# Optimization experiments

Hardware: AMD Instinct MI355X
Metric: run time of the kernel (lower is better)

## Reference

```python
import jax, jax.numpy as jnp
import numpy as np

B, S, D, H, DH, G, C, FF = 4, 4096, 768, 12, 64, 64, 256, 3072


def _ln(x, g, b):
    m = x.mean(-1, keepdims=True)
    v = ((x - m) ** 2).mean(-1, keepdims=True)
    return (x - m) * jax.lax.rsqrt(v + 1e-5) * g + b


def setup_inputs() -> dict:
    key = jax.random.key(0)
    ks = jax.random.split(key, 20)
    w = lambda k, shape: jax.random.normal(k, shape, jnp.float32) * 0.02
    inp = dict(
        cur_input=jax.random.normal(ks[0], (B, S, D), jnp.float32),
        prevLayerOutput=jax.random.normal(ks[1], (B, S, D), jnp.float32),
        classVector=jax.random.normal(ks[2], (B, C), jnp.float32),
        rand_idx=jax.random.randint(ks[3], (B, G), 0, S),
        # self-attention (rand+global) projections
        Wq=w(ks[4], (D, D)), bq=jnp.zeros(D), Wk=w(ks[5], (D, D)), bk=jnp.zeros(D),
        Wv=w(ks[6], (D, D)), bv=jnp.zeros(D), Wo=w(ks[7], (D, D)), bo=jnp.zeros(D),
        g1=jnp.ones(D), b1=jnp.zeros(D),
        # cross-attention over class vector (k/v feature dim is 1 after unsqueeze(-1))
        Wqc=w(ks[8], (D, D)), bqc=jnp.zeros(D), Wkc=w(ks[9], (1, D)), bkc=jnp.zeros(D),
        Wvc=w(ks[10], (1, D)), bvc=jnp.zeros(D), Woc=w(ks[11], (D, D)), boc=jnp.zeros(D),
        g2=jnp.ones(D), b2=jnp.zeros(D),
        # feed-forward
        W1=w(ks[12], (D, FF)), bf1=jnp.zeros(FF), W2=w(ks[13], (FF, D)), bf2=jnp.zeros(D),
        g3=jnp.ones(D), b3=jnp.zeros(D),
    )
    return inp


def reference(cur_input, prevLayerOutput, classVector, rand_idx,
              Wq, bq, Wk, bk, Wv, bv, Wo, bo, g1, b1,
              Wqc, bqc, Wkc, bkc, Wvc, bvc, Woc, boc, g2, b2,
              W1, bf1, W2, bf2, g3, b3):
    scale = np.float32(1.0 / np.sqrt(DH))
    # ---- masked multi-head self attention over global + random tokens ----
    q = (cur_input @ Wq + bq).reshape(B, S, H, DH)
    k = (prevLayerOutput @ Wk + bk).reshape(B, S, H, DH)
    v = (prevLayerOutput @ Wv + bv).reshape(B, S, H, DH)
    sel = jnp.concatenate([jnp.broadcast_to(jnp.arange(G), (B, G)), rand_idx], axis=1)  # [B,2G]
    idx = jnp.broadcast_to(sel[:, :, None, None], (B, 2 * G, H, DH))
    ksel = jnp.take_along_axis(k, idx, axis=1)  # [B,2G,H,DH]
    vsel = jnp.take_along_axis(v, idx, axis=1)
    scores = jnp.einsum('bshd,bkhd->bhsk', q, ksel) * scale  # [B,H,S,2G]
    mask = sel[:, None, None, :] <= jnp.arange(S)[None, None, :, None]  # causal wrt key position
    scores = jnp.where(mask, scores, jnp.float32(-1e9))
    attn = jax.nn.softmax(scores, axis=-1)
    o = jnp.einsum('bhsk,bkhd->bshd', attn, vsel).reshape(B, S, D) @ Wo + bo
    x1 = _ln(cur_input + o, g1, b1)
    # ---- cross attention over class vector (kv seq = C, kv feat = 1) ----
    cv = classVector[:, :, None]  # [B,C,1]
    qc = (x1 @ Wqc + bqc).reshape(B, S, H, DH)
    kc = (cv @ Wkc + bkc).reshape(B, C, H, DH)
    vc = (cv @ Wvc + bvc).reshape(B, C, H, DH)
    sc = jnp.einsum('bshd,bchd->bhsc', qc, kc) * scale
    ac = jax.nn.softmax(sc, axis=-1)
    oc = jnp.einsum('bhsc,bchd->bshd', ac, vc).reshape(B, S, D) @ Woc + boc
    x2 = _ln(x1 + oc, g2, b2)
    # ---- feed forward ----
    ff = jax.nn.relu(x2 @ W1 + bf1) @ W2 + bf2
    return _ln(x2 + ff, g3, b3)
```

## Files before the change

kernel.cpp:

```cpp
#include <hip/hip_runtime.h>
#include <hip/hip_bf16.h>

#define B_ 4
#define S_ 4096
#define D_ 768
#define H_ 12
#define DH_ 64
#define G_ 64
#define C_ 256
#define FF_ 3072

typedef __attribute__((ext_vector_type(8))) short bf16x8;
typedef __attribute__((ext_vector_type(4))) float f32x4;
typedef unsigned short u16;

__device__ __forceinline__ float bfu2f(u16 u) {
    return __uint_as_float((unsigned)u << 16);
}

__device__ __forceinline__ void gload16(const __hip_bfloat16* g, __hip_bfloat16* l) {
    __builtin_amdgcn_global_load_lds(
        (__attribute__((address_space(1))) void*)(void*)const_cast<__hip_bfloat16*>(g),
        (__attribute__((address_space(3))) void*)(void*)l,
        16, 0, 0);
}

__global__ __launch_bounds__(512, 2) void gemm256(
    const u16* __restrict__ A, const u16* __restrict__ Bt,
    const float* __restrict__ bias, u16* __restrict__ Cb,
    int M, int N, int K, int flags)
{
    __shared__ __attribute__((aligned(16))) u16 Ah[2][2][128 * 64];
    __shared__ __attribute__((aligned(16))) u16 Bh[2][2][128 * 64];

    const int tid = threadIdx.x;
    const int lane = tid & 63, w = tid >> 6;
    const int wm = w >> 2, wn = w & 3;
    const int r = lane & 15, qd = lane >> 4;

    int lin = blockIdx.y * gridDim.x + blockIdx.x;
    int nwg = gridDim.x * gridDim.y;
    int cpx = nwg >> 3;
    int swz = (lin & 7) * cpx + (lin >> 3);
    int bm = (swz / gridDim.x) * 256;
    int bn = (swz % gridDim.x) * 256;

    const int srow = tid >> 3;
    const int scol = ((tid & 7) ^ (srow & 7)) * 8;
    const int sdst = tid * 8;

#define STG_A(c, h, kt) { \
    const u16* s_ = A + (size_t)(bm + (h) * 128 + srow) * K + ((kt) << 6) + scol; \
    gload16((const __hip_bfloat16*)s_, (__hip_bfloat16*)&Ah[c][h][sdst]); \
    gload16((const __hip_bfloat16*)(s_ + (size_t)64 * K), (__hip_bfloat16*)&Ah[c][h][sdst + 4096]); }
#define STG_B(c, h, kt) { \
    const u16* s_ = Bt + (size_t)(bn + (h) * 128 + srow) * K + ((kt) << 6) + scol; \
    gload16((const __hip_bfloat16*)s_, (__hip_bfloat16*)&Bh[c][h][sdst]); \
    gload16((const __hip_bfloat16*)(s_ + (size_t)64 * K), (__hip_bfloat16*)&Bh[c][h][sdst + 4096]); }

#define GRAN(kk) (((((kk) << 2) + qd) ^ (r & 7)) * 8)
#define READS_AF(c, mb) { \
    _Pragma("unroll") for (int m = 0; m < 4; ++m) { \
        const u16* p_ = &Ah[c][wm][((mb + m) * 16 + r) * 64]; \
        af[m][0] = *(const bf16x8*)(p_ + GRAN(0)); \
        af[m][1] = *(const bf16x8*)(p_ + GRAN(1)); } }
#define READS_BF(dst, c, nb) { \
    _Pragma("unroll") for (int n = 0; n < 2; ++n) { \
        const u16* p_ = &Bh[c][wn >> 1][((wn & 1) * 64 + (nb + n) * 16 + r) * 64]; \
        dst[n][0] = *(const bf16x8*)(p_ + GRAN(0)); \
        dst[n][1] = *(const bf16x8*)(p_ + GRAN(1)); } }
#define QMFMA(mb, nb, bfx) { \
    __builtin_amdgcn_s_setprio(1); \
    _Pragma("unroll") for (int kk = 0; kk < 2; ++kk) \
    _Pragma("unroll") for (int m = 0; m < 4; ++m) \
    _Pragma("unroll") for (int n = 0; n < 2; ++n) \
        acc[mb + m][nb + n] = __builtin_amdgcn_mfma_f32_16x16x32_bf16( \
            af[m][kk], bfx[n][kk], acc[mb + m][nb + n], 0, 0, 0); \
    __builtin_amdgcn_s_setprio(0); }
#define BAR() __builtin_amdgcn_s_barrier()
#define LGKM0() asm volatile("s_waitcnt lgkmcnt(0)" ::: "memory")

    f32x4 acc[8][4] = {};
    const int NT = K >> 6;
    const int J = NT >> 1;

    STG_A(0, 0, 0) STG_A(0, 1, 0) STG_B(0, 0, 0) STG_B(0, 1, 0)
    STG_B(1, 0, 1) STG_B(1, 1, 1)
    asm volatile("s_waitcnt vmcnt(4)" ::: "memory");
    BAR();

    bf16x8 af[4][2], bf0[2][2], bf1[2][2];

    for (int j = 0; j < J; ++j) {
        const int to1 = 2 * j + 1;
        const int te2 = 2 * j + 2;
        const int to3 = 2 * j + 3;
        const bool pf = (j < J - 1);

        READS_AF(0, 0) READS_BF(bf0, 0, 0)
        STG_A(1, 0, to1)
        BAR(); LGKM0();
        QMFMA(0, 0, bf0)
        BAR();
        READS_BF(bf1, 0, 2)
        STG_A(1, 1, to1)
        BAR(); LGKM0();
        QMFMA(0, 2, bf1)
        BAR();
        READS_AF(0, 4)
        if (pf) { STG_B(0, 0, te2) }
        BAR(); LGKM0();
        QMFMA(4, 2, bf1)
        BAR();
        if (pf) { STG_B(0, 1, te2) }
        BAR();
        QMFMA(4, 0, bf0)
        if (pf) asm volatile("s_waitcnt vmcnt(4)" ::: "memory");
        else    asm volatile("s_waitcnt vmcnt(0)" ::: "memory");
        BAR();
        READS_AF(1, 0) READS_BF(bf0, 1, 0)
        if (pf) { STG_A(0, 0, te2) }
        BAR(); LGKM0();
        QMFMA(0, 0, bf0)
        BAR();
        READS_BF(bf1, 1, 2)
        if (pf) { STG_A(0, 1, te2) }
        BAR(); LGKM0();
        QMFMA(0, 2, bf1)
        BAR();
        READS_AF(1, 4)
        if (pf) { STG_B(1, 0, to3) }
        BAR(); LGKM0();
        QMFMA(4, 2, bf1)
        BAR();
        if (pf) { STG_B(1, 1, to3) }
        BAR();
        QMFMA(4, 0, bf0)
        if (pf) {
            asm volatile("s_waitcnt vmcnt(4)" ::: "memory");
            BAR();
        }
    }

#pragma unroll
    for (int m = 0; m < 8; ++m) {
        int row0 = bm + wm * 128 + m * 16 + qd * 4;
#pragma unroll
        for (int n = 0; n < 4; ++n) {
            int col = bn + wn * 64 + n * 16 + r;
            float bv = (flags & 1) ? bias[col] : 0.0f;
#pragma unroll
            for (int i = 0; i < 4; ++i) {
                float v = acc[m][n][i] + bv;
                if (flags & 2) v = fmaxf(v, 0.0f);
                __hip_bfloat16 ob = __float2bfloat16(v);
                Cb[(size_t)(row0 + i) * N + col] = *(u16*)&ob;
            }
        }
    }
#undef STG_A
#undef STG_B
#undef GRAN
#undef READS_AF
#undef READS_BF
#undef QMFMA
#undef BAR
#undef LGKM0
}

__global__ __launch_bounds__(256) void gemm_mfma(
    const __hip_bfloat16* __restrict__ A, const __hip_bfloat16* __restrict__ Bt,
    const float* __restrict__ bias, float* __restrict__ Cf,
    __hip_bfloat16* __restrict__ Cb,
    int M, int N, int K, int lda, int ldbt, int flags)
{
    __shared__ __hip_bfloat16 As[2][128 * 32];
    __shared__ __hip_bfloat16 Bs[2][128 * 32];

    const int t = threadIdx.x;
    const int lane = t & 63;
    const int wave = t >> 6;
    const int wr = wave >> 1, wc = wave & 1;
    const int qd = lane >> 4, r = lane & 15;

    int lin = blockIdx.y * gridDim.x + blockIdx.x;
    int nwg = gridDim.x * gridDim.y;
    int cpx = nwg >> 3;
    int swz = (lin & 7) * cpx + (lin >> 3);
    int bm = (swz / gridDim.x) * 128;
    int bn = (swz % gridDim.x) * 128;

    const int srow = lane >> 2;
    const int scol = (lane & 3) * 8;
    const __hip_bfloat16* gA0 = A + (size_t)(bm + wave * 32 + srow) * lda + scol;
    const __hip_bfloat16* gA1 = gA0 + (size_t)16 * lda;
    const __hip_bfloat16* gB0 = Bt + (size_t)(bn + wave * 32 + srow) * ldbt + scol;
    const __hip_bfloat16* gB1 = gB0 + (size_t)16 * ldbt;

    f32x4 acc[4][4] = {};

    gload16(gA0, &As[0][wave * 1024]);
    gload16(gA1, &As[0][wave * 1024 + 512]);
    gload16(gB0, &Bs[0][wave * 1024]);
    gload16(gB1, &Bs[0][wave * 1024 + 512]);
    __syncthreads();

    int cur = 0;
    for (int k0 = 0; k0 < K; k0 += 32, cur ^= 1) {
        if (k0 + 32 < K) {
            int kn = k0 + 32, nb = cur ^ 1;
            gload16(gA0 + kn, &As[nb][wave * 1024]);
            gload16(gA1 + kn, &As[nb][wave * 1024 + 512]);
            gload16(gB0 + kn, &Bs[nb][wave * 1024]);
            gload16(gB1 + kn, &Bs[nb][wave * 1024 + 512]);
        }
        bf16x8 afr[4], bfr[4];
#pragma unroll
        for (int m = 0; m < 4; ++m)
            afr[m] = *(const bf16x8*)&As[cur][(wr * 64 + m * 16 + r) * 32 + qd * 8];
#pragma unroll
        for (int n = 0; n < 4; ++n)
            bfr[n] = *(const bf16x8*)&Bs[cur][(wc * 64 + n * 16 + r) * 32 + qd * 8];
#pragma unroll
        for (int m = 0; m < 4; ++m)
#pragma unroll
            for (int n = 0; n < 4; ++n)
                acc[m][n] = __builtin_amdgcn_mfma_f32_16x16x32_bf16(
                    afr[m], bfr[n], acc[m][n], 0, 0, 0);
        __syncthreads();
    }

#pragma unroll
    for (int m = 0; m < 4; ++m) {
        int row0 = bm + wr * 64 + m * 16 + qd * 4;
#pragma unroll
        for (int n = 0; n < 4; ++n) {
            int col = bn + wc * 64 + n * 16 + r;
            float bv = (flags & 1) ? bias[col] : 0.0f;
#pragma unroll
            for (int i = 0; i < 4; ++i) {
                float v = acc[m][n][i] + bv;
                if (flags & 2) v = fmaxf(v, 0.0f);
                size_t off = (size_t)(row0 + i) * N + col;
                if (flags & 4) v += Cf[off];
                if (flags & 8) Cb[off] = __float2bfloat16(v);
                else           Cf[off] = v;
            }
        }
    }
}

__global__ __launch_bounds__(256) void conv_bf16(const float* __restrict__ in,
                                                 __hip_bfloat16* __restrict__ out,
                                                 int n8)
{
    int i = blockIdx.x * 256 + threadIdx.x;
    if (i >= n8) return;
    const float4* p = (const float4*)(in + (size_t)i * 8);
    float4 v0 = p[0], v1 = p[1];
    __hip_bfloat16 o[8] = {
        __float2bfloat16(v0.x), __float2bfloat16(v0.y),
        __float2bfloat16(v0.z), __float2bfloat16(v0.w),
        __float2bfloat16(v1.x), __float2bfloat16(v1.y),
        __float2bfloat16(v1.z), __float2bfloat16(v1.w)};
    *(uint4*)(out + (size_t)i * 8) = *(const uint4*)o;
}

__global__ __launch_bounds__(256) void transp_all(
    const float* __restrict__ Wq, const float* __restrict__ Wo,
    const float* __restrict__ Wk, const float* __restrict__ Wv,
    const float* __restrict__ W1, const float* __restrict__ W2,
    __hip_bfloat16* __restrict__ Wqt, __hip_bfloat16* __restrict__ Wot,
    __hip_bfloat16* __restrict__ Wkt, __hip_bfloat16* __restrict__ Wvt,
    __hip_bfloat16* __restrict__ W1t, __hip_bfloat16* __restrict__ W2t)
{
    int tile = blockIdx.x;
    const float* W; __hip_bfloat16* Wt; int K, N;
    if (tile < 2304) {
        int w = tile / 576; tile -= w * 576;
        K = 768; N = 768;
        W  = (w == 0) ? Wq : (w == 1) ? Wo : (w == 2) ? Wk : Wv;
        Wt = (w == 0) ? Wqt : (w == 1) ? Wot : (w == 2) ? Wkt : Wvt;
    } else if (tile < 4608) { tile -= 2304; K = 768; N = 3072; W = W1; Wt = W1t; }
    else                    { tile -= 4608; K = 3072; N = 768; W = W2; Wt = W2t; }
    int ntx = N >> 5;
    int k0 = (tile / ntx) * 32, n0 = (tile % ntx) * 32;
    __shared__ float s[32][33];
    int tx = threadIdx.x & 31, ty = threadIdx.x >> 5;
#pragma unroll
    for (int i = 0; i < 4; ++i)
        s[ty + i * 8][tx] = W[(size_t)(k0 + ty + i * 8) * N + n0 + tx];
    __syncthreads();
#pragma unroll
    for (int i = 0; i < 4; ++i)
        Wt[(size_t)(n0 + ty + i * 8) * K + k0 + tx] =
            __float2bfloat16(s[tx][ty + i * 8]);
}

__global__ void gather_kernel(const float* __restrict__ prev,
                              const int* __restrict__ rand_idx,
                              __hip_bfloat16* __restrict__ Pselb,
                              int* __restrict__ sel)
{
    int j = blockIdx.x;
    int b = j >> 7, i = j & 127;
    int sv = (i < 64) ? i : rand_idx[b * G_ + (i - 64)];
    if (threadIdx.x == 0) sel[j] = sv;
    const float* src = prev + ((size_t)(b * S_ + sv)) * D_;
    __hip_bfloat16* dst = Pselb + (size_t)j * D_;
    for (int d = threadIdx.x; d < D_; d += blockDim.x)
        dst[d] = __float2bfloat16(src[d]);
}

__global__ __launch_bounds__(256) void attn3_kernel(
    const u16* __restrict__ qb, const u16* __restrict__ kb,
    const u16* __restrict__ vb, const int* __restrict__ sel,
    u16* __restrict__ out)
{
    const int bh = blockIdx.y;
    const int b = bh / H_, h = bh % H_;
    const int s0 = blockIdx.x * 256;
    const int t = threadIdx.x;
    const int w = t >> 6, lane = t & 63;
    const int r = lane & 15, qd = lane >> 4;

    __shared__ u16 Vt[64][136];
    __shared__ u16 Plds[4][32][136];
    __shared__ int ssel[128];

    {
        int key0 = t >> 4;
        int d0 = (t & 15) * 4;
        for (int kk = key0; kk < 128; kk += 16) {
            ushort4 v = *(const ushort4*)(vb + (size_t)(b * 128 + kk) * D_ + h * 64 + d0);
            Vt[d0 + 0][kk] = v.x; Vt[d0 + 1][kk] = v.y;
            Vt[d0 + 2][kk] = v.z; Vt[d0 + 3][kk] = v.w;
        }
        if (t < 128) ssel[t] = sel[b * 128 + t];
    }
    __syncthreads();

    int selv[8];
#pragma unroll
    for (int n = 0; n < 8; ++n) selv[n] = ssel[n * 16 + r];

    for (int pass = 0; pass < 2; ++pass) {
        const int sbase = s0 + w * 64 + pass * 32;
        f32x4 accs[2][8] = {};

#pragma unroll
        for (int ks = 0; ks < 2; ++ks) {
            bf16x8 af[2];
#pragma unroll
            for (int m = 0; m < 2; ++m)
                af[m] = *(const bf16x8*)(qb + (size_t)(b * S_ + sbase + m * 16 + r) * D_ + h * 64 + ks * 32 + qd * 8);
#pragma unroll
            for (int n = 0; n < 8; ++n) {
                bf16x8 bfv = *(const bf16x8*)(kb + (size_t)(b * 128 + n * 16 + r) * D_ + h * 64 + ks * 32 + qd * 8);
#pragma unroll
                for (int m = 0; m < 2; ++m)
                    accs[m][n] = __builtin_amdgcn_mfma_f32_16x16x32_bf16(
                        af[m], bfv, accs[m][n], 0, 0, 0);
            }
        }

#pragma unroll
        for (int m = 0; m < 2; ++m) {
#pragma unroll
            for (int i = 0; i < 4; ++i) {
                int srow = sbase + m * 16 + qd * 4 + i;
                float pm = -3e38f;
#pragma unroll
                for (int n = 0; n < 8; ++n) {
                    float sc = accs[m][n][i] * 0.125f;
                    if (selv[n] > srow) sc = -1e9f;
                    accs[m][n][i] = sc;
                    pm = fmaxf(pm, sc);
                }
#pragma unroll
                for (int off = 1; off < 16; off <<= 1)
                    pm = fmaxf(pm, __shfl_xor(pm, off, 64));
                float ps = 0.f;
#pragma unroll
                for (int n = 0; n < 8; ++n) {
                    float e = __expf(accs[m][n][i] - pm);
                    accs[m][n][i] = e;
                    ps += e;
                }
#pragma unroll
                for (int off = 1; off < 16; off <<= 1)
                    ps += __shfl_xor(ps, off, 64);
                float inv = 1.0f / ps;
#pragma unroll
                for (int n = 0; n < 8; ++n)
                    accs[m][n][i] *= inv;
            }
        }

#pragma unroll
        for (int m = 0; m < 2; ++m)
#pragma unroll
            for (int n = 0; n < 8; ++n)
#pragma unroll
                for (int i = 0; i < 4; ++i) {
                    __hip_bfloat16 pb = __float2bfloat16(accs[m][n][i]);
                    Plds[w][m * 16 + qd * 4 + i][n * 16 + r] = *(u16*)&pb;
                }

        f32x4 acco[2][4] = {};
#pragma unroll
        for (int ks = 0; ks < 4; ++ks) {
            bf16x8 pa[2];
#pragma unroll
            for (int m = 0; m < 2; ++m)
                pa[m] = *(const bf16x8*)&Plds[w][m * 16 + r][ks * 32 + qd * 8];
#pragma unroll
            for (int nd = 0; nd < 4; ++nd) {
                bf16x8 bv = *(const bf16x8*)&Vt[nd * 16 + r][ks * 32 + qd * 8];
#pragma unroll
                for (int m = 0; m < 2; ++m)
                    acco[m][nd] = __builtin_amdgcn_mfma_f32_16x16x32_bf16(
                        pa[m], bv, acco[m][nd], 0, 0, 0);
            }
        }

#pragma unroll
        for (int m = 0; m < 2; ++m)
#pragma unroll
            for (int nd = 0; nd < 4; ++nd)
#pragma unroll
                for (int i = 0; i < 4; ++i) {
                    __hip_bfloat16 ob = __float2bfloat16(acco[m][nd][i]);
                    out[(size_t)(b * S_ + sbase + m * 16 + qd * 4 + i) * D_ + h * 64 + nd * 16 + r] = *(u16*)&ob;
                }
    }
}

__global__ __launch_bounds__(192) void addln_bb(
    const u16* __restrict__ xa, const u16* __restrict__ xb,
    const float* __restrict__ g, const float* __restrict__ beta,
    float* __restrict__ out)
{
    const int row = blockIdx.x;
    const int t = threadIdx.x;
    const ushort4 a = ((const ushort4*)(xa + (size_t)row * D_))[t];
    const ushort4 b4 = ((const ushort4*)(xb + (size_t)row * D_))[t];
    float v[4] = {bfu2f(a.x) + bfu2f(b4.x), bfu2f(a.y) + bfu2f(b4.y),
                  bfu2f(a.z) + bfu2f(b4.z), bfu2f(a.w) + bfu2f(b4.w)};
    float sum = v[0] + v[1] + v[2] + v[3];
#pragma unroll
    for (int off = 1; off < 64; off <<= 1) sum += __shfl_xor(sum, off, 64);
    __shared__ float r1[3], r2[3];
    int wv = t >> 6, ln = t & 63;
    if (ln == 0) r1[wv] = sum;
    __syncthreads();
    float mean = (r1[0] + r1[1] + r1[2]) * (1.0f / 768.0f);
    float sq = 0.f;
#pragma unroll
    for (int i = 0; i < 4; ++i) { v[i] -= mean; sq += v[i] * v[i]; }
#pragma unroll
    for (int off = 1; off < 64; off <<= 1) sq += __shfl_xor(sq, off, 64);
    if (ln == 0) r2[wv] = sq;
    __syncthreads();
    float var = (r2[0] + r2[1] + r2[2]) * (1.0f / 768.0f);
    float rs = rsqrtf(var + 1e-5f);
    float4 gg = ((const float4*)g)[t];
    float4 bb = ((const float4*)beta)[t];
    float4 o;
    o.x = v[0] * rs * gg.x + bb.x;
    o.y = v[1] * rs * gg.y + bb.y;
    o.z = v[2] * rs * gg.z + bb.z;
    o.w = v[3] * rs * gg.w + bb.w;
    ((float4*)(out + (size_t)row * D_))[t] = o;
}

__global__ __launch_bounds__(256) void precompute_U(
    const float* __restrict__ Wqc, const float* __restrict__ Wkc,
    const float* __restrict__ bqc, float* __restrict__ Ut, float* __restrict__ ab)
{
    __shared__ __attribute__((aligned(16))) float wk[D_];
    for (int i = threadIdx.x; i < D_; i += 256) wk[i] = Wkc[i];
    __syncthreads();
    int idx = blockIdx.x * 256 + threadIdx.x;
    int h = idx / D_, d = idx - h * D_;
    const float4* row = (const float4*)(Wqc + (size_t)d * D_ + h * 64);
    const float4* wkv = (const float4*)(wk + h * 64);
    float a0 = 0.f, a1 = 0.f, a2 = 0.f, a3 = 0.f;
#pragma unroll
    for (int j = 0; j < 16; j += 4) {
        float4 r0 = row[j], r1 = row[j + 1], r2 = row[j + 2], r3 = row[j + 3];
        float4 c0 = wkv[j], c1 = wkv[j + 1], c2 = wkv[j + 2], c3 = wkv[j + 3];
        a0 += r0.x * c0.x + r0.y * c0.y + r0.z * c0.z + r0.w * c0.w;
        a1 += r1.x * c1.x + r1.y * c1.y + r1.z * c1.z + r1.w * c1.w;
        a2 += r2.x * c2.x + r2.y * c2.y + r2.z * c2.z + r2.w * c2.w;
        a3 += r3.x * c3.x + r3.y * c3.y + r3.z * c3.z + r3.w * c3.w;
    }
    Ut[idx] = (a0 + a1) + (a2 + a3);
    if (idx < H_) {
        const float4* bq4 = (const float4*)(bqc + idx * 64);
        const float4* wk4 = (const float4*)(wk + idx * 64);
        float s = 0.f;
#pragma unroll
        for (int j = 0; j < 16; ++j) {
            float4 bb = bq4[j], cc = wk4[j];
            s += bb.x * cc.x + bb.y * cc.y + bb.z * cc.z + bb.w * cc.w;
        }
        ab[idx] = s;
    }
}

__global__ __launch_bounds__(256) void precompute_mix(
    const float* __restrict__ Wvc, const float* __restrict__ Woc,
    float* __restrict__ Wmix)
{
    __shared__ float wv[D_];
    for (int i = threadIdx.x; i < D_; i += 256) wv[i] = Wvc[i];
    __syncthreads();
    int idx = blockIdx.x * 256 + threadIdx.x;
    int h = idx / D_, n = idx - h * D_;
    float acc[8] = {};
#pragma unroll
    for (int j = 0; j < 64; ++j)
        acc[j & 7] += wv[h * 64 + j] * Woc[(size_t)(h * 64 + j) * D_ + n];
    Wmix[idx] = ((acc[0] + acc[1]) + (acc[2] + acc[3]))
              + ((acc[4] + acc[5]) + (acc[6] + acc[7]));
}

__global__ __launch_bounds__(256) void precompute_bias2(
    const float* __restrict__ Woc, const float* __restrict__ bvc,
    const float* __restrict__ boc, float* __restrict__ bias2)
{
    int tx = threadIdx.x & 63, ty = threadIdx.x >> 6;
    int n = blockIdx.x * 64 + tx;
    int d0 = ty * 192;
    float a = 0.f;
#pragma unroll 8
    for (int d = 0; d < 192; ++d)
        a += bvc[d0 + d] * Woc[(size_t)(d0 + d) * D_ + n];
    __shared__ float red[4][64];
    red[ty][tx] = a;
    __syncthreads();
    if (ty == 0)
        bias2[n] = boc[n] + red[0][tx] + red[1][tx] + red[2][tx] + red[3][tx];
}

__global__ __launch_bounds__(256) void fused_mid(
    const float* __restrict__ cur, const u16* __restrict__ oprojb,
    const float* __restrict__ g1, const float* __restrict__ b1,
    const float* __restrict__ Ut, const float* __restrict__ ab,
    const float* __restrict__ cvec,
    const float* __restrict__ Wmix, const float* __restrict__ bias2,
    const float* __restrict__ g2, const float* __restrict__ b2,
    __hip_bfloat16* __restrict__ x2b)
{
    const int w = threadIdx.x >> 6, lane = threadIdx.x & 63;
    const int row0 = blockIdx.x * 8 + w * 2;
    const int b = blockIdx.x >> 9;

    __shared__ float4 cvs[64];
    __shared__ float xp[4][64][28];
    __shared__ float muls[4][24];

    if (threadIdx.x < 64)
        cvs[threadIdx.x] = ((const float4*)(cvec + b * C_))[threadIdx.x];

    float4 x1[2][3];
#pragma unroll
    for (int rr = 0; rr < 2; ++rr) {
        const float4* pa = (const float4*)(cur + (size_t)(row0 + rr) * D_);
        const ushort4* pb = (const ushort4*)(oprojb + (size_t)(row0 + rr) * D_);
        float s = 0.f;
#pragma unroll
        for (int i = 0; i < 3; ++i) {
            float4 a = pa[i * 64 + lane];
            ushort4 ou = pb[i * 64 + lane];
            float4 v;
            v.x = a.x + bfu2f(ou.x); v.y = a.y + bfu2f(ou.y);
            v.z = a.z + bfu2f(ou.z); v.w = a.w + bfu2f(ou.w);
            x1[rr][i] = v;
            s += v.x + v.y + v.z + v.w;
        }
#pragma unroll
        for (int off = 1; off < 64; off <<= 1) s += __shfl_xor(s, off, 64);
        float mean = s * (1.0f / 768.0f);
        float sq = 0.f;
#pragma unroll
        for (int i = 0; i < 3; ++i) {
            x1[rr][i].x -= mean; x1[rr][i].y -= mean;
            x1[rr][i].z -= mean; x1[rr][i].w -= mean;
            sq += x1[rr][i].x * x1[rr][i].x + x1[rr][i].y * x1[rr][i].y
                + x1[rr][i].z * x1[rr][i].z + x1[rr][i].w * x1[rr][i].w;
        }
#pragma unroll
        for (int off = 1; off < 64; off <<= 1) sq += __shfl_xor(sq, off, 64);
        float rs = rsqrtf(sq * (1.0f / 768.0f) + 1e-5f);
#pragma unroll
        for (int i = 0; i < 3; ++i) {
            float4 gg = ((const float4*)g1)[i * 64 + lane];
            float4 bb = ((const float4*)b1)[i * 64 + lane];
            x1[rr][i].x = x1[rr][i].x * rs * gg.x + bb.x;
            x1[rr][i].y = x1[rr][i].y * rs * gg.y + bb.y;
            x1[rr][i].z = x1[rr][i].z * rs * gg.z + bb.z;
            x1[rr][i].w = x1[rr][i].w * rs * gg.w + bb.w;
        }
    }

    float acc[24];
#pragma unroll
    for (int j = 0; j < 24; ++j) acc[j] = 0.f;
#pragma unroll
    for (int i = 0; i < 3; ++i) {
#pragma unroll
        for (int h = 0; h < 12; ++h) {
            float4 u = ((const float4*)(Ut + (size_t)h * D_))[i * 64 + lane];
#pragma unroll
            for (int rr = 0; rr < 2; ++rr)
                acc[rr * 12 + h] += x1[rr][i].x * u.x + x1[rr][i].y * u.y
                                  + x1[rr][i].z * u.z + x1[rr][i].w * u.w;
        }
    }
#pragma unroll
    for (int j4 = 0; j4 < 6; ++j4)
        *(float4*)&xp[w][lane][j4 * 4] = *(float4*)&acc[j4 * 4];
    __syncthreads();

    if (lane < 48) {
        int j = lane >> 1, half = lane & 1;
        float ssum = 0.f;
#pragma unroll
        for (int k = 0; k < 32; ++k) ssum += xp[w][half * 32 + k][j];
        ssum += __shfl_xor(ssum, 1, 64);
        float a = 0.125f * (ssum + ab[j % 12]);
        float z = 0.f, ms = 0.f;
#pragma unroll
        for (int it = 0; it < 32; ++it) {
            float4 c = cvs[half * 32 + it];
            float e0 = __expf(a * c.x), e1 = __expf(a * c.y),
                  e2 = __expf(a * c.z), e3 = __expf(a * c.w);
            z += e0 + e1 + e2 + e3;
            ms += e0 * c.x + e1 * c.y + e2 * c.z + e3 * c.w;
        }
        z += __shfl_xor(z, 1, 64);
        ms += __shfl_xor(ms, 1, 64);
        if (half == 0) muls[w][j] = ms / z;
    }
    __syncthreads();

    float4 t2[2][3];
#pragma unroll
    for (int i = 0; i < 3; ++i) {
        float4 bv = ((const float4*)bias2)[i * 64 + lane];
        float4 o0 = bv, o1 = bv;
#pragma unroll
        for (int h = 0; h < 12; ++h) {
            float4 wm = ((const float4*)(Wmix + (size_t)h * D_))[i * 64 + lane];
            float m0 = muls[w][h], m1 = muls[w][12 + h];
            o0.x += m0 * wm.x; o0.y += m0 * wm.y; o0.z += m0 * wm.z; o0.w += m0 * wm.w;
            o1.x += m1 * wm.x; o1.y += m1 * wm.y; o1.z += m1 * wm.z; o1.w += m1 * wm.w;
        }
        t2[0][i].x = x1[0][i].x + o0.x; t2[0][i].y = x1[0][i].y + o0.y;
        t2[0][i].z = x1[0][i].z + o0.z; t2[0][i].w = x1[0][i].w + o0.w;
        t2[1][i].x = x1[1][i].x + o1.x; t2[1][i].y = x1[1][i].y + o1.y;
        t2[1][i].z = x1[1][i].z + o1.z; t2[1][i].w = x1[1][i].w + o1.w;
    }

#pragma unroll
    for (int rr = 0; rr < 2; ++rr) {
        float s = 0.f;
#pragma unroll
        for (int i = 0; i < 3; ++i)
            s += t2[rr][i].x + t2[rr][i].y + t2[rr][i].z + t2[rr][i].w;
#pragma unroll
        for (int off = 1; off < 64; off <<= 1) s += __shfl_xor(s, off, 64);
        float mean = s * (1.0f / 768.0f);
        float sq = 0.f;
#pragma unroll
        for (int i = 0; i < 3; ++i) {
            t2[rr][i].x -= mean; t2[rr][i].y -= mean;
            t2[rr][i].z -= mean; t2[rr][i].w -= mean;
            sq += t2[rr][i].x * t2[rr][i].x + t2[rr][i].y * t2[rr][i].y
                + t2[rr][i].z * t2[rr][i].z + t2[rr][i].w * t2[rr][i].w;
        }
#pragma unroll
        for (int off = 1; off < 64; off <<= 1) sq += __shfl_xor(sq, off, 64);
        float rs = rsqrtf(sq * (1.0f / 768.0f) + 1e-5f);
        size_t base = (size_t)(row0 + rr) * D_;
#pragma unroll
        for (int i = 0; i < 3; ++i) {
            float4 gg = ((const float4*)g2)[i * 64 + lane];
            float4 bb = ((const float4*)b2)[i * 64 + lane];
            float vx = t2[rr][i].x * rs * gg.x + bb.x;
            float vy = t2[rr][i].y * rs * gg.y + bb.y;
            float vz = t2[rr][i].z * rs * gg.z + bb.z;
            float vw = t2[rr][i].w * rs * gg.w + bb.w;
            __hip_bfloat16 pk[4] = {
                __float2bfloat16(vx), __float2bfloat16(vy),
                __float2bfloat16(vz), __float2bfloat16(vw)};
            *(uint2*)(x2b + base + i * 256 + lane * 4) = *(const uint2*)pk;
        }
    }
}

extern "C" void kernel_launch(void* const* d_in, const int* in_sizes, int n_in,
                              void* d_out, int out_size, void* d_ws, size_t ws_size,
                              hipStream_t stream) {
    const float* cur   = (const float*)d_in[0];
    const float* prev  = (const float*)d_in[1];
    const float* cvec  = (const float*)d_in[2];
    const int*   ridx  = (const int*)d_in[3];
    const float* Wq  = (const float*)d_in[4];
    const float* bq  = (const float*)d_in[5];
    const float* Wk  = (const float*)d_in[6];
    const float* bk  = (const float*)d_in[7];
    const float* Wv  = (const float*)d_in[8];
    const float* bv  = (const float*)d_in[9];
    const float* Wo  = (const float*)d_in[10];
    const float* bo  = (const float*)d_in[11];
    const float* g1  = (const float*)d_in[12];
    const float* b1  = (const float*)d_in[13];
    const float* Wqc = (const float*)d_in[14];
    const float* bqc = (const float*)d_in[15];
    const float* Wkc = (const float*)d_in[16];
    const float* bkc = (const float*)d_in[17];  (void)bkc;
    const float* Wvc = (const float*)d_in[18];
    const float* bvc = (const float*)d_in[19];
    const float* Woc = (const float*)d_in[20];
    const float* boc = (const float*)d_in[21];
    const float* g2  = (const float*)d_in[22];
    const float* b2  = (const float*)d_in[23];
    const float* W1  = (const float*)d_in[24];
    const float* bf1 = (const float*)d_in[25];
    const float* W2  = (const float*)d_in[26];
    const float* bf2 = (const float*)d_in[27];
    const float* g3  = (const float*)d_in[28];
    const float* b3  = (const float*)d_in[29];
    float* outp = (float*)d_out;
    (void)ws_size; (void)in_sizes; (void)n_in; (void)out_size;

    const int M = B_ * S_;
    const size_t NBSD = (size_t)M * D_;
    const size_t NSEL = (size_t)B_ * 128 * D_;

    __hip_bfloat16* hidb  = (__hip_bfloat16*)d_ws;
    __hip_bfloat16* bf0   = hidb + (size_t)M * FF_;
    __hip_bfloat16* tmpb  = bf0 + NBSD;
    __hip_bfloat16* Pselb = tmpb + NBSD;
    __hip_bfloat16* kselb = Pselb + NSEL;
    __hip_bfloat16* vselb = kselb + NSEL;
    __hip_bfloat16* Wqt   = vselb + NSEL;
    __hip_bfloat16* Wot   = Wqt + (size_t)D_ * D_;
    __hip_bfloat16* Wkt   = Wot + (size_t)D_ * D_;
    __hip_bfloat16* Wvt   = Wkt + (size_t)D_ * D_;
    __hip_bfloat16* W1t   = Wvt + (size_t)D_ * D_;
    __hip_bfloat16* W2t   = W1t + (size_t)D_ * FF_;
    float* Ub    = (float*)(W2t + (size_t)FF_ * D_);
    float* abv   = Ub + (size_t)D_ * H_;
    float* Wmix  = abv + 16;
    float* bias2 = Wmix + (size_t)H_ * D_;
    int*   selb  = (int*)(bias2 + D_);

    gather_kernel<<<B_ * 128, 256, 0, stream>>>(prev, ridx, Pselb, selb);
    transp_all<<<6912, 256, 0, stream>>>(Wq, Wo, Wk, Wv, W1, W2,
                                         Wqt, Wot, Wkt, Wvt, W1t, W2t);
    conv_bf16<<<(int)(NBSD / 8 + 255) / 256, 256, 0, stream>>>(cur, bf0, (int)(NBSD / 8));
    precompute_U<<<36, 256, 0, stream>>>(Wqc, Wkc, bqc, Ub, abv);
    precompute_mix<<<36, 256, 0, stream>>>(Wvc, Woc, Wmix);
    precompute_bias2<<<12, 256, 0, stream>>>(Woc, bvc, boc, bias2);

    {
        dim3 g(D_ / 128, (B_ * 128) / 128);
        gemm_mfma<<<g, 256, 0, stream>>>(Pselb, Wkt, bk, nullptr, kselb,
                                         B_ * 128, D_, D_, D_, D_, 1 | 8);
        gemm_mfma<<<g, 256, 0, stream>>>(Pselb, Wvt, bv, nullptr, vselb,
                                         B_ * 128, D_, D_, D_, D_, 1 | 8);
    }

    gemm256<<<dim3(D_ / 256, M / 256), 512, 0, stream>>>(
        (const u16*)bf0, (const u16*)Wqt, bq, (u16*)tmpb, M, D_, D_, 1);

    attn3_kernel<<<dim3(S_ / 256, B_ * H_), 256, 0, stream>>>(
        (const u16*)tmpb, (const u16*)kselb, (const u16*)vselb, selb, (u16*)bf0);

    gemm256<<<dim3(D_ / 256, M / 256), 512, 0, stream>>>(
        (const u16*)bf0, (const u16*)Wot, bo, (u16*)tmpb, M, D_, D_, 1);

    fused_mid<<<M / 8, 256, 0, stream>>>(
        cur, (const u16*)tmpb, g1, b1, Ub, abv, cvec, Wmix, bias2, g2, b2, bf0);

    gemm256<<<dim3(FF_ / 256, M / 256), 512, 0, stream>>>(
        (const u16*)bf0, (const u16*)W1t, bf1, (u16*)hidb, M, FF_, D_, 1 | 2);
    gemm256<<<dim3(D_ / 256, M / 256), 512, 0, stream>>>(
        (const u16*)hidb, (const u16*)W2t, bf2, (u16*)tmpb, M, D_, FF_, 1);

    addln_bb<<<M, 192, 0, stream>>>((const u16*)bf0, (const u16*)tmpb, g3, b3, outp);
}
```

Baseline: 438.3 us.

## Reorder gemm256 LDS prefetch schedule and read bf16 residual in fused_mid

Restructures the gemm256 main loop so LDS fragment reads for the next MFMA block are issued right after the current MFMA batch, and swaps which A/B half-tiles are staged in each phase, removing some barriers. Fragments for the next iteration are preloaded before the loop ends. Separately, attention output goes to the hidb buffer so the bf16 copy of cur_input stays in bf0, and fused_mid reads that bf16 residual instead of fp32 cur, halving its residual read traffic at the cost of bf16 precision on the residual. fused_mid reads and writes bf0 in place, which works only if each block touches only its own rows.

```diff
diff --git a/kernel.cpp b/kernel.cpp
--- a/kernel.cpp
+++ b/kernel.cpp
@@ -84,61 +84,58 @@
     const int NT = K >> 6;
     const int J = NT >> 1;
 
+    bf16x8 af[4][2], bfa[2][2], bfb[2][2];
+
     STG_A(0, 0, 0) STG_A(0, 1, 0) STG_B(0, 0, 0) STG_B(0, 1, 0)
-    STG_B(1, 0, 1) STG_B(1, 1, 1)
+    STG_A(1, 0, 1) STG_A(1, 1, 1)
     asm volatile("s_waitcnt vmcnt(4)" ::: "memory");
     BAR();
-
-    bf16x8 af[4][2], bf0[2][2], bf1[2][2];
+    READS_AF(0, 0) READS_BF(bfa, 0, 0)
 
     for (int j = 0; j < J; ++j) {
-        const int to1 = 2 * j + 1;
-        const int te2 = 2 * j + 2;
-        const int to3 = 2 * j + 3;
-        const bool pf = (j < J - 1);
-
-        READS_AF(0, 0) READS_BF(bf0, 0, 0)
-        STG_A(1, 0, to1)
+        const int to1 = 2 * j + 1, te2 = 2 * j + 2, to3 = 2 * j + 3;
+        const bool pf = (j + 1 < J);
+
+        STG_B(1, 0, to1)
         BAR(); LGKM0();
-        QMFMA(0, 0, bf0)
-        BAR();
-        READS_BF(bf1, 0, 2)
-        STG_A(1, 1, to1)
+        QMFMA(0, 0, bfa)
+        READS_BF(bfb, 0, 2)
+        BAR();
+        STG_B(1, 1, to1)
         BAR(); LGKM0();
-        QMFMA(0, 2, bf1)
-        BAR();
+        QMFMA(0, 2, bfb)
         READS_AF(0, 4)
+        BAR();
+        LGKM0();
+        QMFMA(4, 2, bfb)
+        BAR();
+        if (pf) { STG_A(0, 0, te2) STG_A(0, 1, te2) }
+        BAR();
+        QMFMA(4, 0, bfa)
+        if (pf) asm volatile("s_waitcnt vmcnt(4)" ::: "memory");
+        else    asm volatile("s_waitcnt vmcnt(0)" ::: "memory");
+        BAR();
+        READS_AF(1, 0) READS_BF(bfa, 1, 0)
         if (pf) { STG_B(0, 0, te2) }
         BAR(); LGKM0();
-        QMFMA(4, 2, bf1)
+        QMFMA(0, 0, bfa)
+        READS_BF(bfb, 1, 2)
         BAR();
         if (pf) { STG_B(0, 1, te2) }
-        BAR();
-        QMFMA(4, 0, bf0)
-        if (pf) asm volatile("s_waitcnt vmcnt(4)" ::: "memory");
-        else    asm volatile("s_waitcnt vmcnt(0)" ::: "memory");
-        BAR();
-        READS_AF(1, 0) READS_BF(bf0, 1, 0)
-        if (pf) { STG_A(0, 0, te2) }
         BAR(); LGKM0();
-        QMFMA(0, 0, bf0)
-        BAR();
-        READS_BF(bf1, 1, 2)
-        if (pf) { STG_A(0, 1, te2) }
-        BAR(); LGKM0();
-        QMFMA(0, 2, bf1)
-        BAR();
+        QMFMA(0, 2, bfb)
         READS_AF(1, 4)
-        if (pf) { STG_B(1, 0, to3) }
-        BAR(); LGKM0();
-        QMFMA(4, 2, bf1)
-        BAR();
-        if (pf) { STG_B(1, 1, to3) }
-        BAR();
-        QMFMA(4, 0, bf0)
+        BAR();
+        LGKM0();
+        QMFMA(4, 2, bfb)
+        BAR();
+        if (pf) { STG_A(1, 0, to3) STG_A(1, 1, to3) }
+        BAR();
+        QMFMA(4, 0, bfa)
         if (pf) {
             asm volatile("s_waitcnt vmcnt(4)" ::: "memory");
             BAR();
+            READS_AF(0, 0) READS_BF(bfa, 0, 0)
         }
     }
 
@@ -545,7 +542,7 @@
 }
 
 __global__ __launch_bounds__(256) void fused_mid(
-    const float* __restrict__ cur, const u16* __restrict__ oprojb,
+    const u16* __restrict__ curb, const u16* __restrict__ oprojb,
     const float* __restrict__ g1, const float* __restrict__ b1,
     const float* __restrict__ Ut, const float* __restrict__ ab,
     const float* __restrict__ cvec,
@@ -567,16 +564,16 @@
     float4 x1[2][3];
 #pragma unroll
     for (int rr = 0; rr < 2; ++rr) {
-        const float4* pa = (const float4*)(cur + (size_t)(row0 + rr) * D_);
+        const ushort4* pa = (const ushort4*)(curb + (size_t)(row0 + rr) * D_);
         const ushort4* pb = (const ushort4*)(oprojb + (size_t)(row0 + rr) * D_);
         float s = 0.f;
 #pragma unroll
         for (int i = 0; i < 3; ++i) {
-            float4 a = pa[i * 64 + lane];
+            ushort4 au = pa[i * 64 + lane];
             ushort4 ou = pb[i * 64 + lane];
             float4 v;
-            v.x = a.x + bfu2f(ou.x); v.y = a.y + bfu2f(ou.y);
-            v.z = a.z + bfu2f(ou.z); v.w = a.w + bfu2f(ou.w);
+            v.x = bfu2f(au.x) + bfu2f(ou.x); v.y = bfu2f(au.y) + bfu2f(ou.y);
+            v.z = bfu2f(au.z) + bfu2f(ou.z); v.w = bfu2f(au.w) + bfu2f(ou.w);
             x1[rr][i] = v;
             s += v.x + v.y + v.z + v.w;
         }
@@ -779,13 +776,14 @@
         (const u16*)bf0, (const u16*)Wqt, bq, (u16*)tmpb, M, D_, D_, 1);
 
     attn3_kernel<<<dim3(S_ / 256, B_ * H_), 256, 0, stream>>>(
-        (const u16*)tmpb, (const u16*)kselb, (const u16*)vselb, selb, (u16*)bf0);
+        (const u16*)tmpb, (const u16*)kselb, (const u16*)vselb, selb, (u16*)hidb);
 
     gemm256<<<dim3(D_ / 256, M / 256), 512, 0, stream>>>(
-        (const u16*)bf0, (const u16*)Wot, bo, (u16*)tmpb, M, D_, D_, 1);
+        (const u16*)hidb, (const u16*)Wot, bo, (u16*)tmpb, M, D_, D_, 1);
 
     fused_mid<<<M / 8, 256, 0, stream>>>(
-        cur, (const u16*)tmpb, g1, b1, Ub, abv, cvec, Wmix, bias2, g2, b2, bf0);
+        (const u16*)bf0, (const u16*)tmpb, g1, b1, Ub, abv, cvec, Wmix, bias2,
+        g2, b2, bf0);
 
     gemm256<<<dim3(FF_ / 256, M / 256), 512, 0, stream>>>(
         (const u16*)bf0, (const u16*)W1t, bf1, (u16*)hidb, M, FF_, D_, 1 | 2);
```

Measured after the change: 430.8 us. No clear change (-1.7%).
